# Performance work log

Hardware: AMD Instinct MI355X
Metric: run time of the kernel (lower is better)

## Reference

```python
import jax, jax.numpy as jnp
import numpy as np

B, T, N, FI = 2, 16, 256, 1
H, NHEAD, L = 64, 4, 2
MID, LOW, FOUT = 32, 16, 1


def layer_norm(x, g, b, eps=1e-5):
    m = jnp.mean(x, axis=-1, keepdims=True)
    v = jnp.var(x, axis=-1, keepdims=True)
    return (x - m) / jnp.sqrt(v + eps) * g + b


def setup_inputs() -> dict:
    key = jax.random.key(0)
    ks = jax.random.split(key, 24)
    s = 0.05
    inp = {
        'x_seq': jax.random.normal(ks[0], (B, T, N, FI), jnp.float32),
        'edge_index': jax.random.randint(ks[1], (2, 16), 0, N),
        'Wi': jax.random.normal(ks[2], (FI, H), jnp.float32) * s,
        'bi': jnp.zeros((H,), jnp.float32),
        'Wqkv': jax.random.normal(ks[3], (L, H, 3 * H), jnp.float32) * s,
        'bqkv': jnp.zeros((L, 3 * H), jnp.float32),
        'Wo': jax.random.normal(ks[4], (L, H, H), jnp.float32) * s,
        'bo': jnp.zeros((L, H), jnp.float32),
        'ln1_g': jnp.ones((L, H), jnp.float32),
        'ln1_b': jnp.zeros((L, H), jnp.float32),
        'W1': jax.random.normal(ks[5], (L, H, 4 * H), jnp.float32) * s,
        'b1': jnp.zeros((L, 4 * H), jnp.float32),
        'W2': jax.random.normal(ks[6], (L, 4 * H, H), jnp.float32) * s,
        'b2': jnp.zeros((L, H), jnp.float32),
        'ln2_g': jnp.ones((L, H), jnp.float32),
        'ln2_b': jnp.zeros((L, H), jnp.float32),
        'dW1': jax.random.normal(ks[7], (H, MID), jnp.float32) * s,
        'db1': jnp.zeros((MID,), jnp.float32),
        'dW2': jax.random.normal(ks[8], (MID, LOW), jnp.float32) * s,
        'db2': jnp.zeros((LOW,), jnp.float32),
        'dW3': jax.random.normal(ks[9], (LOW, FOUT), jnp.float32) * s,
        'db3': jnp.zeros((FOUT,), jnp.float32),
    }
    return inp


def reference(x_seq, edge_index, Wi, bi, Wqkv, bqkv, Wo, bo, ln1_g, ln1_b,
              W1, b1, W2, b2, ln2_g, ln2_b, dW1, db1, dW2, db2, dW3, db3):
    b, t, n, _ = x_seq.shape
    dh = H // NHEAD
    # input projection
    x = x_seq @ Wi + bi  # [B,T,N,H]
    # sinusoidal time positional encoding (broadcast over nodes)
    pos = jnp.arange(t, dtype=jnp.float32)[:, None]
    div = jnp.exp(jnp.arange(0, H, 2, dtype=jnp.float32) * (-jnp.log(10000.0) / H))
    tp = jnp.zeros((t, H), jnp.float32)
    tp = tp.at[:, 0::2].set(jnp.sin(pos * div)).at[:, 1::2].set(jnp.cos(pos * div))
    x = x + tp[None, :, None, :]
    S = t * n
    x = x.reshape(b, S, H)
    # block-causal additive bias: position i cannot attend to strictly future timesteps
    t_idx = jnp.arange(S) // n
    bias = jnp.where(t_idx[None, :] > t_idx[:, None], -jnp.inf, 0.0).astype(x.dtype)
    inv_sqrt_dh = 1.0 / jnp.sqrt(jnp.asarray(dh, x.dtype))
    for l in range(L):
        qkv = x @ Wqkv[l] + bqkv[l]  # [B,S,3H]
        q, k, v = jnp.split(qkv, 3, axis=-1)
        q = q.reshape(b, S, NHEAD, dh).transpose(0, 2, 1, 3)
        k = k.reshape(b, S, NHEAD, dh).transpose(0, 2, 1, 3)
        v = v.reshape(b, S, NHEAD, dh).transpose(0, 2, 1, 3)
        scores = jnp.einsum('bhqd,bhkd->bhqk', q, k) * inv_sqrt_dh + bias
        attn = jax.nn.softmax(scores, axis=-1)
        o = jnp.einsum('bhqk,bhkd->bhqd', attn, v)
        o = o.transpose(0, 2, 1, 3).reshape(b, S, H)
        o = o @ Wo[l] + bo[l]
        x = layer_norm(x + o, ln1_g[l], ln1_b[l])
        f = jax.nn.relu(x @ W1[l] + b1[l]) @ W2[l] + b2[l]
        x = layer_norm(x + f, ln2_g[l], ln2_b[l])
    last = x.reshape(b, t, n, H)[:, -1]  # [B,N,H]
    h = jax.nn.relu(last @ dW1 + db1)
    h = jax.nn.relu(h @ dW2 + db2)
    return h @ dW3 + db3  # [B,N,1]
```

## Files before the change

kernel.cpp:

```cpp
#include <hip/hip_runtime.h>
#include <math.h>


namespace {
constexpr int T_ = 16, N_ = 256, S_ = 4096;
constexpr int PAIRS = 136;

constexpr size_t OFF_A    = 0;
constexpr size_t OFF_BT   = 192;
constexpr size_t OFF_XB   = 3264;
constexpr size_t OFF_ALPH = 4288;
constexpr size_t OFF_BET  = 4292;
constexpr size_t OFF_GAM  = 4356;
constexpr size_t OFF_DELT = 4420;
constexpr size_t OFF_MN   = 5444;
constexpr size_t OFF_MX   = 5476;
constexpr size_t OFF_X    = 5632;
constexpr size_t OFF_QKV  = 529920;
constexpr size_t OFF_P0   = 2102784;
constexpr size_t OFF_PM1  = 3675648;
constexpr size_t OFF_PL1  = 3708416;
constexpr size_t OFF_PA1  = 3741184;
constexpr size_t OFF_WT   = 4265472;

typedef float  f32x16 __attribute__((ext_vector_type(16)));
typedef short  short8 __attribute__((ext_vector_type(8)));

__device__ inline float wave_sum(float v) {
#pragma unroll
  for (int off = 32; off > 0; off >>= 1) v += __shfl_xor(v, off, 64);
  return v;
}
__device__ inline unsigned bf16_rne(float f) {
  unsigned u = __float_as_uint(f);
  return (u + 0x7FFFu + ((u >> 16) & 1u)) >> 16;
}
__device__ inline unsigned pack2(float a, float b) {
  return bf16_rne(a) | (bf16_rne(b) << 16);
}
__device__ inline f32x16 zero16() {
  f32x16 z;
#pragma unroll
  for (int i = 0; i < 16; ++i) z[i] = 0.f;
  return z;
}
__device__ inline float pe_val(int t, int h) {
  float div = __expf((float)(h & ~1) * (-0.14391156831212787f));
  float arg = (float)t * div;
  return (h & 1) ? cosf(arg) : sinf(arg);
}
__device__ inline float rebuild(short h, short l) {
  return __uint_as_float(((unsigned)(unsigned short)h) << 16) +
         __uint_as_float(((unsigned)(unsigned short)l) << 16);
}
__device__ __forceinline__ void split4_store(short* hp, short* lp,
                                             float v0, float v1, float v2, float v3) {
  unsigned u0 = __float_as_uint(v0), u1 = __float_as_uint(v1);
  unsigned u2 = __float_as_uint(v2), u3 = __float_as_uint(v3);
  float r0 = v0 - __uint_as_float(u0 & 0xFFFF0000u);
  float r1 = v1 - __uint_as_float(u1 & 0xFFFF0000u);
  float r2 = v2 - __uint_as_float(u2 & 0xFFFF0000u);
  float r3 = v3 - __uint_as_float(u3 & 0xFFFF0000u);
  *(uint2*)hp = make_uint2((u0 >> 16) | (u1 & 0xFFFF0000u),
                           (u2 >> 16) | (u3 & 0xFFFF0000u));
  *(uint2*)lp = make_uint2(pack2(r0, r1), pack2(r2, r3));
}
__device__ __forceinline__ f32x16 gemm_tile(
    const short* __restrict__ Wh, const short* __restrict__ Wl, int tileRow,
    int inDim, int nkt, const short* Bh, const short* Bl, int bstride,
    int l31, int hi) {
  f32x16 C = zero16();
  for (int kt = 0; kt < nkt; ++kt) {
    int ko = kt * 16 + 8 * hi;
    short8 Ah = *(const short8*)&Wh[tileRow * inDim + ko];
    short8 Al = *(const short8*)&Wl[tileRow * inDim + ko];
    short8 Bh8 = *(const short8*)&Bh[l31 * bstride + ko];
    short8 Bl8 = *(const short8*)&Bl[l31 * bstride + ko];
    C = __builtin_amdgcn_mfma_f32_32x32x16_bf16(Ah, Bh8, C, 0, 0, 0);
    C = __builtin_amdgcn_mfma_f32_32x32x16_bf16(Al, Bh8, C, 0, 0, 0);
    C = __builtin_amdgcn_mfma_f32_32x32x16_bf16(Ah, Bl8, C, 0, 0, 0);
  }
  return C;
}

__global__ void k_setup(const float* __restrict__ x_seq,
                        const float* __restrict__ Wi, const float* __restrict__ bi,
                        const float* __restrict__ Wqkv, const float* __restrict__ bqkv,
                        const float* __restrict__ Wo, const float* __restrict__ W1,
                        const float* __restrict__ W2,
                        float* __restrict__ A, float* __restrict__ Bt,
                        float* __restrict__ Xb,
                        float* __restrict__ ALPH, float* __restrict__ BET,
                        float* __restrict__ GAM, float* __restrict__ DELT,
                        float* __restrict__ MN, float* __restrict__ MX,
                        short* __restrict__ WT) {
  int t = blockIdx.x, tid = threadIdx.x;
  if (t < 16) {
    if (tid < 192) {
      float acc = bqkv[tid];
#pragma unroll 8
      for (int h = 0; h < 64; ++h)
        acc = fmaf(bi[h] + pe_val(t, h), Wqkv[h * 192 + tid], acc);
      Bt[t * 192 + tid] = acc;
    }
    if (tid < 64) Xb[t * 64 + tid] = bi[tid] + pe_val(t, tid);
  } else if (t == 16) {
    if (tid < 192) {
      float acc = 0.f;
#pragma unroll 8
      for (int h = 0; h < 64; ++h) acc = fmaf(Wi[h], Wqkv[h * 192 + tid], acc);
      A[tid] = acc;
    }
  } else if (t == 17) {
    __shared__ float sA[128];
    __shared__ float sB[16][128];
    if (tid < 128) {
      float acc = 0.f;
#pragma unroll 8
      for (int h = 0; h < 64; ++h) acc = fmaf(Wi[h], Wqkv[h * 192 + tid], acc);
      sA[tid] = acc;
    }
    {
      int tt = tid >> 4, i = tid & 15;
      float accv[8];
#pragma unroll
      for (int j = 0; j < 8; ++j) accv[j] = bqkv[i * 8 + j];
      for (int h = 0; h < 64; ++h) {
        float xb = bi[h] + pe_val(tt, h);
#pragma unroll
        for (int j = 0; j < 8; ++j)
          accv[j] = fmaf(xb, Wqkv[h * 192 + i * 8 + j], accv[j]);
      }
#pragma unroll
      for (int j = 0; j < 8; ++j) sB[tt][i * 8 + j] = accv[j];
    }
    __syncthreads();
    const float k2 = 0.36067376022224085f;
    if (tid < 4) {
      float d = 0.f;
#pragma unroll
      for (int i = 0; i < 16; ++i) d = fmaf(sA[tid * 16 + i], sA[64 + tid * 16 + i], d);
      ALPH[tid] = k2 * d;
    }
    if (tid < 64) {
      int h = tid >> 4, tp2 = tid & 15;
      float d = 0.f, g = 0.f;
#pragma unroll
      for (int i = 0; i < 16; ++i) {
        d = fmaf(sA[h * 16 + i], sB[tp2][64 + h * 16 + i], d);
        g = fmaf(sA[64 + h * 16 + i], sB[tp2][h * 16 + i], g);
      }
      BET[h * 16 + tp2] = k2 * d;
      GAM[h * 16 + tp2] = k2 * g;
    }
#pragma unroll
    for (int q = 0; q < 4; ++q) {
      int idx = tid + 256 * q;
      int h = idx >> 8, ta = (idx >> 4) & 15, tb = idx & 15;
      float d = 0.f;
#pragma unroll
      for (int i = 0; i < 16; ++i)
        d = fmaf(sB[ta][h * 16 + i], sB[tb][64 + h * 16 + i], d);
      DELT[h * 256 + ta * 16 + tb] = k2 * d;
    }
  } else if (t == 18) {
    int g = tid >> 3, i = tid & 7;
    const float* xp = x_seq + (g >> 4) * S_ + (g & 15) * N_;
    float mn = 1e30f, mx = -1e30f;
    for (int j = i; j < 256; j += 8) {
      float v = xp[j];
      mn = fminf(mn, v); mx = fmaxf(mx, v);
    }
#pragma unroll
    for (int off = 1; off < 8; off <<= 1) {
      mn = fminf(mn, __shfl_xor(mn, off, 64));
      mx = fmaxf(mx, __shfl_xor(mx, off, 64));
    }
    if (i == 0) { MN[g] = mn; MX[g] = mx; }
  } else {
    int tb2 = t - 19;
    const float* Wq1 = Wqkv + 64 * 192;
#pragma unroll
    for (int e = 0; e < 4; ++e) {
      int gi = tb2 * 1024 + e * 256 + tid;
      float v; int hdst, ldst;
      if (gi < 4096) {
        int o = gi >> 6, i = gi & 63; v = Wo[i * 64 + o];
        hdst = gi; ldst = gi + 4096;
      } else if (gi < 20480) {
        int li = gi - 4096; int o = li >> 6, i = li & 63; v = W1[i * 256 + o];
        hdst = 8192 + li; ldst = 24576 + li;
      } else if (gi < 36864) {
        int li = gi - 20480; int o = li >> 8, i = li & 255; v = W2[i * 64 + o];
        hdst = 40960 + li; ldst = 57344 + li;
      } else {
        int li = gi - 36864; int o = li >> 6, i = li & 63; v = Wq1[i * 192 + o];
        hdst = 73728 + li; ldst = 86016 + li;
      }
      unsigned u = __float_as_uint(v);
      WT[hdst] = (short)(u >> 16);
      WT[ldst] = (short)bf16_rne(v - __uint_as_float(u & 0xFFFF0000u));
    }
  }
}

__global__ __launch_bounds__(256, 4) void k_attn0(
    const float* __restrict__ x_seq,
    const float* __restrict__ ALPH, const float* __restrict__ BET,
    const float* __restrict__ GAM, const float* __restrict__ DELT,
    const float* __restrict__ MN, const float* __restrict__ MX,
    float* __restrict__ P0) {
  __shared__ float4 xk4[64];
  int blk = blockIdx.x;
  int bh = blk / PAIRS, pair = blk % PAIRS;
  int b = bh >> 2, h = bh & 3;
  int tq = 0, p = pair;
  while (p >= tq + 1) { p -= tq + 1; ++tq; }
  int kt = p;
  int tid = threadIdx.x;
  if (tid < 64) xk4[tid] = *(const float4*)(x_seq + (size_t)(b * S_ + kt * N_) + 4 * tid);
  __syncthreads();

  float x = x_seq[b * S_ + tq * N_ + tid];
  float a = fmaf(ALPH[h], x, GAM[h * 16 + tq]);
  float xext = (a >= 0.f) ? MX[b * 16 + kt] : MN[b * 16 + kt];
  float axext = a * xext;
  float Mg = axext + fmaf(BET[h * 16 + kt], x, DELT[h * 256 + tq * 16 + kt]);
  float sp0 = 0.f, sp1 = 0.f, sp2 = 0.f, sp3 = 0.f;
  float sx0 = 0.f, sx1 = 0.f, sx2 = 0.f, sx3 = 0.f;
#pragma unroll 8
  for (int j = 0; j < 64; ++j) {
    float4 xv = xk4[j];
    float e0 = __builtin_amdgcn_exp2f(fmaf(a, xv.x, -axext));
    float e1 = __builtin_amdgcn_exp2f(fmaf(a, xv.y, -axext));
    float e2 = __builtin_amdgcn_exp2f(fmaf(a, xv.z, -axext));
    float e3 = __builtin_amdgcn_exp2f(fmaf(a, xv.w, -axext));
    sp0 += e0; sp1 += e1; sp2 += e2; sp3 += e3;
    sx0 = fmaf(xv.x, e0, sx0); sx1 = fmaf(xv.y, e1, sx1);
    sx2 = fmaf(xv.z, e2, sx2); sx3 = fmaf(xv.w, e3, sx3);
  }
  size_t pb = ((size_t)(bh * 16 + tq) * 16 + kt) * 768;
  P0[pb + tid]       = Mg;
  P0[pb + 256 + tid] = (sp0 + sp1) + (sp2 + sp3);
  P0[pb + 512 + tid] = (sx0 + sx1) + (sx2 + sx3);
}

__global__ __launch_bounds__(256, 2) void k_fused0(
    const float* __restrict__ P0, const float* __restrict__ A,
    const float* __restrict__ Bt, const float* __restrict__ Xb,
    const float* __restrict__ x_seq, const float* __restrict__ Wi,
    const float* __restrict__ bo, const float* __restrict__ g1,
    const float* __restrict__ be1, const float* __restrict__ bb1,
    const float* __restrict__ bb2, const float* __restrict__ g2,
    const float* __restrict__ be2, const float* __restrict__ bq1,
    const short* __restrict__ WT,
    float* __restrict__ X, float* __restrict__ QKV) {
  __shared__ short qbh[32][72], qbl[32][72];
  __shared__ short xsh[32][72], xsl[32][72];
  __shared__ short hsh[32][264], hsl[32][264];
  __shared__ float ys[16][68];

  const short* WoTh = WT;          const short* WoTl = WT + 4096;
  const short* W1Th = WT + 8192;   const short* W1Tl = WT + 24576;
  const short* W2Th = WT + 40960;  const short* W2Tl = WT + 57344;
  const short* WqTh = WT + 73728;  const short* WqTl = WT + 86016;

  int blk = blockIdx.x;
  int b = blk >> 8, t = (blk >> 4) & 15, n0 = (blk & 15) * 16;
  int gbase = b * S_ + t * N_ + n0;
  int tid = threadIdx.x;
  int w = tid >> 6, lane = tid & 63, l31 = lane & 31, hi = lane >> 5;

  for (int i = tid; i < 16 * 72; i += 256) {
    (&qbh[16][0])[i] = 0; (&qbl[16][0])[i] = 0;
    (&xsh[16][0])[i] = 0; (&xsl[16][0])[i] = 0;
  }
  for (int i = tid; i < 16 * 264; i += 256) {
    (&hsh[16][0])[i] = 0; (&hsl[16][0])[i] = 0;
  }

  {
    int r = tid & 15, hh = (tid >> 4) & 3, d4 = tid >> 6;
    int n = n0 + r, bh4 = b * 4 + hh;
    size_t pbase = ((size_t)(bh4 * 16 + t) * 16) * 768 + n;
    float M = -INFINITY;
    for (int kt = 0; kt <= t; ++kt)
      M = fmaxf(M, P0[pbase + (size_t)kt * 768]);
    float D = 0.f, SX = 0.f, c0 = 0.f, c1 = 0.f, c2 = 0.f, c3 = 0.f;
    for (int kt = 0; kt <= t; ++kt) {
      size_t pb = pbase + (size_t)kt * 768;
      float wgt = __builtin_amdgcn_exp2f(P0[pb] - M);
      float wsp = wgt * P0[pb + 256];
      D += wsp;
      SX = fmaf(wgt, P0[pb + 512], SX);
      float4 bv = *(const float4*)(Bt + kt * 192 + 128 + hh * 16 + d4 * 4);
      c0 = fmaf(wsp, bv.x, c0); c1 = fmaf(wsp, bv.y, c1);
      c2 = fmaf(wsp, bv.z, c2); c3 = fmaf(wsp, bv.w, c3);
    }
    float invD = 1.f / D;
    float4 av = *(const float4*)(A + 128 + hh * 16 + d4 * 4);
    float o0 = fmaf(SX, av.x, c0) * invD;
    float o1 = fmaf(SX, av.y, c1) * invD;
    float o2 = fmaf(SX, av.z, c2) * invD;
    float o3 = fmaf(SX, av.w, c3) * invD;
    split4_store(&qbh[r][hh * 16 + d4 * 4], &qbl[r][hh * 16 + d4 * 4],
                 o0, o1, o2, o3);
  }
  __syncthreads();

  if (w < 2) {
    f32x16 C = gemm_tile(WoTh, WoTl, w * 32 + l31, 64, 4,
                         &qbh[0][0], &qbl[0][0], 72, l31, hi);
    if (l31 < 16) {
#pragma unroll
      for (int g = 0; g < 4; ++g)
        *(float4*)&ys[l31][w * 32 + g * 8 + 4 * hi] =
            make_float4(C[4 * g], C[4 * g + 1], C[4 * g + 2], C[4 * g + 3]);
    }
  }
  __syncthreads();

  {
    int c = tid & 63, grp = tid >> 6;
    float xb_c = Xb[t * 64 + c], wi_c = Wi[c], bo_c = bo[c];
    float g1c = g1[c], be1c = be1[c];
#pragma unroll
    for (int rr = 0; rr < 4; ++rr) {
      int row = grp * 4 + rr;
      float xv = x_seq[gbase + row];
      float val = ys[row][c] + bo_c + fmaf(xv, wi_c, xb_c);
      float mean = wave_sum(val) * (1.f / 64.f);
      float dv = val - mean;
      float var = wave_sum(dv * dv) * (1.f / 64.f);
      float xn = dv * rsqrtf(var + 1e-5f) * g1c + be1c;
      unsigned u = __float_as_uint(xn);
      xsh[row][c] = (short)(u >> 16);
      xsl[row][c] = (short)bf16_rne(xn - __uint_as_float(u & 0xFFFF0000u));
    }
  }
  __syncthreads();

#pragma unroll
  for (int ti = 0; ti < 2; ++ti) {
    int tt = w + 4 * ti;
    f32x16 C = gemm_tile(W1Th, W1Tl, tt * 32 + l31, 64, 4,
                         &xsh[0][0], &xsl[0][0], 72, l31, hi);
    if (l31 < 16) {
#pragma unroll
      for (int g = 0; g < 4; ++g) {
        int cb = tt * 32 + g * 8 + 4 * hi;
        float v0 = fmaxf(C[4 * g + 0] + bb1[cb + 0], 0.f);
        float v1 = fmaxf(C[4 * g + 1] + bb1[cb + 1], 0.f);
        float v2 = fmaxf(C[4 * g + 2] + bb1[cb + 2], 0.f);
        float v3 = fmaxf(C[4 * g + 3] + bb1[cb + 3], 0.f);
        split4_store(&hsh[l31][cb], &hsl[l31][cb], v0, v1, v2, v3);
      }
    }
  }
  __syncthreads();

  if (w < 2) {
    f32x16 C = gemm_tile(W2Th, W2Tl, w * 32 + l31, 256, 16,
                         &hsh[0][0], &hsl[0][0], 264, l31, hi);
    if (l31 < 16) {
#pragma unroll
      for (int g = 0; g < 4; ++g)
        *(float4*)&ys[l31][w * 32 + g * 8 + 4 * hi] =
            make_float4(C[4 * g], C[4 * g + 1], C[4 * g + 2], C[4 * g + 3]);
    }
  }
  __syncthreads();

  {
    int c = tid & 63, grp = tid >> 6;
    float b2c = bb2[c], g2c = g2[c], be2c = be2[c];
#pragma unroll
    for (int rr = 0; rr < 4; ++rr) {
      int row = grp * 4 + rr;
      float val = ys[row][c] + b2c + rebuild(xsh[row][c], xsl[row][c]);
      float mean = wave_sum(val) * (1.f / 64.f);
      float dv = val - mean;
      float var = wave_sum(dv * dv) * (1.f / 64.f);
      float xn = dv * rsqrtf(var + 1e-5f) * g2c + be2c;
      unsigned u = __float_as_uint(xn);
      qbh[row][c] = (short)(u >> 16);
      qbl[row][c] = (short)bf16_rne(xn - __uint_as_float(u & 0xFFFF0000u));
      if (t == 15) X[(size_t)(gbase + row) * 64 + c] = xn;
    }
  }
  __syncthreads();

  {
    int tlA = (t == 15) ? w : (2 + w);
    int ntl = (t == 15 && w < 2) ? 2 : 1;
    for (int ti = 0; ti < ntl; ++ti) {
      int tt = ti ? (w + 4) : tlA;
      f32x16 C = gemm_tile(WqTh, WqTl, tt * 32 + l31, 64, 4,
                           &qbh[0][0], &qbl[0][0], 72, l31, hi);
      if (l31 < 16) {
        size_t rb = (size_t)(gbase + l31) * 192;
#pragma unroll
        for (int g = 0; g < 4; ++g) {
          int cb = tt * 32 + g * 8 + 4 * hi;
          float4 o = make_float4(C[4 * g + 0] + bq1[cb + 0],
                                 C[4 * g + 1] + bq1[cb + 1],
                                 C[4 * g + 2] + bq1[cb + 2],
                                 C[4 * g + 3] + bq1[cb + 3]);
          *(float4*)&QKV[rb + cb] = o;
        }
      }
    }
  }
}

__global__ __launch_bounds__(256, 4) void k_attn1(const float* __restrict__ QKV,
    float* __restrict__ PM, float* __restrict__ PL, float* __restrict__ PACC) {
  __shared__ short KH[2][256][8];
  __shared__ short KL[2][256][8];
  __shared__ short VT[32][264];
  int blk = blockIdx.x;
  int bh = blk >> 4, kt = blk & 15;
  const int tq = 15;
  int b = bh >> 2, h = bh & 3;
  int tid = threadIdx.x, w = tid >> 6, lane = tid & 63;
  int l31 = lane & 31, hi = lane >> 5;
  const size_t qkvbase = (size_t)b * S_ * 192;

  for (int i = tid; i < 16 * 264; i += 256) (&VT[16][0])[i] = 0;
  {
    const float* kp = QKV + qkvbase + (size_t)(kt * N_ + tid) * 192 + 64 + h * 16;
    float kf[16], vf[16];
#pragma unroll
    for (int i = 0; i < 4; ++i) {
      float4 k4 = *(const float4*)(kp + 4 * i);
      kf[4 * i] = k4.x; kf[4 * i + 1] = k4.y; kf[4 * i + 2] = k4.z; kf[4 * i + 3] = k4.w;
      float4 v4 = *(const float4*)(kp + 64 + 4 * i);
      vf[4 * i] = v4.x; vf[4 * i + 1] = v4.y; vf[4 * i + 2] = v4.z; vf[4 * i + 3] = v4.w;
    }
    short8 kh0, kh1, kl0, kl1;
#pragma unroll
    for (int i = 0; i < 8; ++i) {
      unsigned ht0 = __float_as_uint(kf[i]) & 0xFFFF0000u;
      kh0[i] = (short)(ht0 >> 16);
      kl0[i] = (short)bf16_rne(kf[i] - __uint_as_float(ht0));
      unsigned ht1 = __float_as_uint(kf[i + 8]) & 0xFFFF0000u;
      kh1[i] = (short)(ht1 >> 16);
      kl1[i] = (short)bf16_rne(kf[i + 8] - __uint_as_float(ht1));
    }
    *(short8*)&KH[0][tid][0] = kh0;
    *(short8*)&KH[1][tid][0] = kh1;
    *(short8*)&KL[0][tid][0] = kl0;
    *(short8*)&KL[1][tid][0] = kl1;
#pragma unroll
    for (int i = 0; i < 16; ++i) VT[i][tid] = (short)bf16_rne(vf[i]);
  }
  __syncthreads();

  const float cscale = 0.36067376022224085f;
  short8 Qh[2], Ql[2];
#pragma unroll
  for (int qs = 0; qs < 2; ++qs) {
    int qloc = w * 64 + qs * 32 + l31;
    const float* qp = QKV + qkvbase + (size_t)(tq * N_ + qloc) * 192 + h * 16 + 8 * hi;
    float4 a4 = *(const float4*)(qp), b4 = *(const float4*)(qp + 4);
    float qf[8] = {a4.x, a4.y, a4.z, a4.w, b4.x, b4.y, b4.z, b4.w};
#pragma unroll
    for (int i = 0; i < 8; ++i) {
      float q = qf[i] * cscale;
      unsigned ht = __float_as_uint(q) & 0xFFFF0000u;
      Qh[qs][i] = (short)(ht >> 16);
      Ql[qs][i] = (short)bf16_rne(q - __uint_as_float(ht));
    }
  }

  f32x16 O0 = zero16(), O1 = zero16();
  float m[2] = {-INFINITY, -INFINITY}, lsum[2] = {0.f, 0.f};

  for (int ks = 0; ks < 8; ++ks) {
    const short8 Kh = *(const short8*)&KH[hi][ks * 32 + l31][0];
    const short8 Kl = *(const short8*)&KL[hi][ks * 32 + l31][0];
    const short8 Va = *(const short8*)&VT[l31][ks * 32 + 8 * hi];
    const short8 Vb = *(const short8*)&VT[l31][ks * 32 + 8 * hi + 16];

#pragma unroll
    for (int qs = 0; qs < 2; ++qs) {
      f32x16 S = zero16();
      S = __builtin_amdgcn_mfma_f32_32x32x16_bf16(Kh, Qh[qs], S, 0, 0, 0);
      S = __builtin_amdgcn_mfma_f32_32x32x16_bf16(Kl, Qh[qs], S, 0, 0, 0);
      S = __builtin_amdgcn_mfma_f32_32x32x16_bf16(Kh, Ql[qs], S, 0, 0, 0);

      float pm = S[0];
#pragma unroll
      for (int r = 1; r < 16; ++r) pm = fmaxf(pm, S[r]);
      pm = fmaxf(pm, __shfl_xor(pm, 32, 64));
      float mq = m[qs];
      if (__any(pm > mq)) {
        float mn = fmaxf(mq, pm);
        float al = __builtin_amdgcn_exp2f(mq - mn);
        m[qs] = mn; mq = mn;
        lsum[qs] *= al;
        if (qs == 0) {
#pragma unroll
          for (int r = 0; r < 16; ++r) O0[r] *= al;
        } else {
#pragma unroll
          for (int r = 0; r < 16; ++r) O1[r] *= al;
        }
      }
      float pr[16], ps = 0.f;
#pragma unroll
      for (int r = 0; r < 16; ++r) {
        pr[r] = __builtin_amdgcn_exp2f(S[r] - mq);
        ps += pr[r];
      }
      lsum[qs] += ps + __shfl_xor(ps, 32, 64);

      unsigned w01 = pack2(pr[0],  pr[1]);
      unsigned w23 = pack2(pr[2],  pr[3]);
      unsigned w45 = pack2(pr[4],  pr[5]);
      unsigned w67 = pack2(pr[6],  pr[7]);
      unsigned w89 = pack2(pr[8],  pr[9]);
      unsigned wab = pack2(pr[10], pr[11]);
      unsigned wcd = pack2(pr[12], pr[13]);
      unsigned wef = pack2(pr[14], pr[15]);
      unsigned e01 = __shfl_xor(w01, 32, 64), e23 = __shfl_xor(w23, 32, 64);
      unsigned e45 = __shfl_xor(w45, 32, 64), e67 = __shfl_xor(w67, 32, 64);
      unsigned e89 = __shfl_xor(w89, 32, 64), eab = __shfl_xor(wab, 32, 64);
      unsigned ecd = __shfl_xor(wcd, 32, 64), eef = __shfl_xor(wef, 32, 64);
      union { short8 s; unsigned u[4]; } P0u, P1u;
      P0u.u[0] = hi ? e45 : w01;
      P0u.u[1] = hi ? e67 : w23;
      P0u.u[2] = hi ? w45 : e01;
      P0u.u[3] = hi ? w67 : e23;
      P1u.u[0] = hi ? ecd : w89;
      P1u.u[1] = hi ? eef : wab;
      P1u.u[2] = hi ? wcd : e89;
      P1u.u[3] = hi ? wef : eab;

      if (qs == 0) {
        O0 = __builtin_amdgcn_mfma_f32_32x32x16_bf16(Va, P0u.s, O0, 0, 0, 0);
        O0 = __builtin_amdgcn_mfma_f32_32x32x16_bf16(Vb, P1u.s, O0, 0, 0, 0);
      } else {
        O1 = __builtin_amdgcn_mfma_f32_32x32x16_bf16(Va, P0u.s, O1, 0, 0, 0);
        O1 = __builtin_amdgcn_mfma_f32_32x32x16_bf16(Vb, P1u.s, O1, 0, 0, 0);
      }
    }
  }

  int slot = blk;
#pragma unroll
  for (int qs = 0; qs < 2; ++qs) {
    int qloc = w * 64 + qs * 32 + l31;
    if (lane < 32) {
      PM[(size_t)slot * 256 + qloc] = m[qs];
      PL[(size_t)slot * 256 + qloc] = lsum[qs];
    }
    float* pa = PACC + (size_t)slot * 4096 + (size_t)qloc * 16;
    float4 lo4, hi4;
    if (qs == 0) {
      lo4 = make_float4(O0[0], O0[1], O0[2], O0[3]);
      hi4 = make_float4(O0[4], O0[5], O0[6], O0[7]);
    } else {
      lo4 = make_float4(O1[0], O1[1], O1[2], O1[3]);
      hi4 = make_float4(O1[4], O1[5], O1[6], O1[7]);
    }
    *(float4*)(pa + 4 * hi)     = lo4;
    *(float4*)(pa + 8 + 4 * hi) = hi4;
  }
}

__global__ __launch_bounds__(256, 2) void k_fused1(
    const float* __restrict__ PM1, const float* __restrict__ PL1,
    const float* __restrict__ PA1,
    const float* __restrict__ Wo, const float* __restrict__ bo,
    const float* __restrict__ g1, const float* __restrict__ be1,
    const float* __restrict__ W1, const float* __restrict__ bb1,
    const float* __restrict__ W2, const float* __restrict__ bb2,
    const float* __restrict__ g2, const float* __restrict__ be2,
    const float* __restrict__ X,
    const float* __restrict__ dW1, const float* __restrict__ db1,
    const float* __restrict__ dW2, const float* __restrict__ db2,
    const float* __restrict__ dW3, const float* __restrict__ db3,
    float* __restrict__ out) {
  __shared__ float os[4][64], rs[4][64], xs[4][64], x2[4][64], hs[4][256];
  __shared__ float h1s[4][32], h2s[4][16];
  int tid = threadIdx.x;
  int bb = blockIdx.x >> 6;
  int nbase = (blockIdx.x & 63) * 4;
  int row0 = bb * S_ + 15 * N_ + nbase;
  size_t base = (size_t)row0 * 64;

  {
    int d = tid & 15, r = (tid >> 4) & 3, h = tid >> 6;
    int n = nbase + r;
    int sb = (bb * 4 + h) * 16;
    float M = -INFINITY;
#pragma unroll
    for (int s = 0; s < 16; ++s) M = fmaxf(M, PM1[(size_t)(sb + s) * 256 + n]);
    float D = 0.f, od = 0.f;
#pragma unroll
    for (int s = 0; s < 16; ++s) {
      float wgt = __builtin_amdgcn_exp2f(PM1[(size_t)(sb + s) * 256 + n] - M);
      D = fmaf(PL1[(size_t)(sb + s) * 256 + n], wgt, D);
      od = fmaf(PA1[(size_t)(sb + s) * 4096 + (size_t)n * 16 + d], wgt, od);
    }
    os[r][h * 16 + d] = od / D;
    rs[tid >> 6][tid & 63] = X[base + tid];
  }
  __syncthreads();

  int c = tid & 63, grp = tid >> 6;
  {
    float a = bo[c];
#pragma unroll 8
    for (int k = 0; k < 64; ++k) a = fmaf(os[grp][k], Wo[k * 64 + c], a);
    float val = a + rs[grp][c];
    float mean = wave_sum(val) * (1.f / 64.f);
    float dv = val - mean;
    float var = wave_sum(dv * dv) * (1.f / 64.f);
    xs[grp][c] = dv * rsqrtf(var + 1e-5f) * g1[c] + be1[c];
  }
  __syncthreads();

  {
    float am0 = bb1[tid], am1 = am0, am2 = am0, am3 = am0;
    for (int k4 = 0; k4 < 16; ++k4) {
      float w0 = W1[(4 * k4 + 0) * 256 + tid];
      float w1v = W1[(4 * k4 + 1) * 256 + tid];
      float w2v = W1[(4 * k4 + 2) * 256 + tid];
      float w3v = W1[(4 * k4 + 3) * 256 + tid];
      float4 x0 = *(const float4*)&xs[0][4 * k4];
      float4 x1 = *(const float4*)&xs[1][4 * k4];
      float4 x2v = *(const float4*)&xs[2][4 * k4];
      float4 x3 = *(const float4*)&xs[3][4 * k4];
      am0 = fmaf(x0.x, w0, am0); am0 = fmaf(x0.y, w1v, am0);
      am0 = fmaf(x0.z, w2v, am0); am0 = fmaf(x0.w, w3v, am0);
      am1 = fmaf(x1.x, w0, am1); am1 = fmaf(x1.y, w1v, am1);
      am1 = fmaf(x1.z, w2v, am1); am1 = fmaf(x1.w, w3v, am1);
      am2 = fmaf(x2v.x, w0, am2); am2 = fmaf(x2v.y, w1v, am2);
      am2 = fmaf(x2v.z, w2v, am2); am2 = fmaf(x2v.w, w3v, am2);
      am3 = fmaf(x3.x, w0, am3); am3 = fmaf(x3.y, w1v, am3);
      am3 = fmaf(x3.z, w2v, am3); am3 = fmaf(x3.w, w3v, am3);
    }
    hs[0][tid] = fmaxf(am0, 0.f);
    hs[1][tid] = fmaxf(am1, 0.f);
    hs[2][tid] = fmaxf(am2, 0.f);
    hs[3][tid] = fmaxf(am3, 0.f);
  }
  __syncthreads();

  {
    float a = bb2[c];
    for (int k4 = 0; k4 < 64; ++k4) {
      float w0 = W2[(4 * k4 + 0) * 64 + c];
      float w1v = W2[(4 * k4 + 1) * 64 + c];
      float w2v = W2[(4 * k4 + 2) * 64 + c];
      float w3v = W2[(4 * k4 + 3) * 64 + c];
      float4 hv = *(const float4*)&hs[grp][4 * k4];
      a = fmaf(hv.x, w0, a); a = fmaf(hv.y, w1v, a);
      a = fmaf(hv.z, w2v, a); a = fmaf(hv.w, w3v, a);
    }
    float val = a + xs[grp][c];
    float mean = wave_sum(val) * (1.f / 64.f);
    float dv = val - mean;
    float var = wave_sum(dv * dv) * (1.f / 64.f);
    x2[grp][c] = dv * rsqrtf(var + 1e-5f) * g2[c] + be2[c];
  }
  __syncthreads();

  if (tid < 128) {
    int r = tid >> 5, mid = tid & 31;
    float a = db1[mid];
#pragma unroll 8
    for (int k = 0; k < 64; ++k) a = fmaf(x2[r][k], dW1[k * 32 + mid], a);
    h1s[r][mid] = fmaxf(a, 0.f);
  }
  __syncthreads();
  if (tid < 64) {
    int r = tid >> 4, low = tid & 15;
    float a = db2[low];
#pragma unroll
    for (int k = 0; k < 32; ++k) a = fmaf(h1s[r][k], dW2[k * 16 + low], a);
    h2s[r][low] = fmaxf(a, 0.f);
  }
  __syncthreads();
  if (tid < 4) {
    float a = db3[0];
#pragma unroll
    for (int k = 0; k < 16; ++k) a = fmaf(h2s[tid][k], dW3[k], a);
    out[bb * 256 + nbase + tid] = a;
  }
}

}

extern "C" void kernel_launch(void* const* d_in, const int* in_sizes, int n_in,
                              void* d_out, int out_size, void* d_ws, size_t ws_size,
                              hipStream_t stream) {
  const float* x_seq = (const float*)d_in[0];
  const float* Wi   = (const float*)d_in[2];
  const float* bi   = (const float*)d_in[3];
  const float* Wqkv = (const float*)d_in[4];
  const float* bqkv = (const float*)d_in[5];
  const float* Wo   = (const float*)d_in[6];
  const float* bo   = (const float*)d_in[7];
  const float* ln1g = (const float*)d_in[8];
  const float* ln1b = (const float*)d_in[9];
  const float* W1   = (const float*)d_in[10];
  const float* b1   = (const float*)d_in[11];
  const float* W2   = (const float*)d_in[12];
  const float* b2   = (const float*)d_in[13];
  const float* ln2g = (const float*)d_in[14];
  const float* ln2b = (const float*)d_in[15];
  const float* dW1  = (const float*)d_in[16];
  const float* db1  = (const float*)d_in[17];
  const float* dW2  = (const float*)d_in[18];
  const float* db2  = (const float*)d_in[19];
  const float* dW3  = (const float*)d_in[20];
  const float* db3  = (const float*)d_in[21];

  float* ws   = (float*)d_ws;
  float* A    = ws + OFF_A;
  float* Bt   = ws + OFF_BT;
  float* Xb   = ws + OFF_XB;
  float* ALPH = ws + OFF_ALPH;
  float* BET  = ws + OFF_BET;
  float* GAM  = ws + OFF_GAM;
  float* DELT = ws + OFF_DELT;
  float* MN   = ws + OFF_MN;
  float* MX   = ws + OFF_MX;
  float* X    = ws + OFF_X;
  float* QKV  = ws + OFF_QKV;
  float* P0   = ws + OFF_P0;
  float* PM1  = ws + OFF_PM1;
  float* PL1  = ws + OFF_PL1;
  float* PA1  = ws + OFF_PA1;
  short* WT   = (short*)(ws + OFF_WT);

  k_setup<<<67, 256, 0, stream>>>(x_seq, Wi, bi, Wqkv, bqkv, Wo, W1, W2,
                                  A, Bt, Xb, ALPH, BET, GAM, DELT, MN, MX, WT);
  k_attn0<<<8 * PAIRS, 256, 0, stream>>>(x_seq, ALPH, BET, GAM, DELT, MN, MX, P0);
  k_fused0<<<512, 256, 0, stream>>>(P0, A, Bt, Xb, x_seq, Wi,
                                    bo, ln1g, ln1b, b1, b2, ln2g, ln2b,
                                    bqkv + 192, WT, X, QKV);
  k_attn1<<<128, 256, 0, stream>>>(QKV, PM1, PL1, PA1);
  k_fused1<<<128, 256, 0, stream>>>(PM1, PL1, PA1,
                                    Wo + 4096, bo + 64, ln1g + 64, ln1b + 64,
                                    W1 + 64 * 256, b1 + 256, W2 + 256 * 64, b2 + 64,
                                    ln2g + 64, ln2b + 64, X,
                                    dW1, db1, dW2, db2, dW3, db3, (float*)d_out);
}
```

Before: 86.24 us.

## Fuse setup kernel into layer-0 attention kernel by recomputing per-block scalars

Removes the separate setup launch by folding its weight-transpose and bias work into extra blocks of the layer-0 attention kernel. Each attention block now computes its own alpha/beta/gamma/delta coefficients and key min/max in-block, instead of reading them from a precomputed workspace. This drops one kernel launch and its dependency barrier. In exchange every attention block does redundant 64-step dot products and extra syncs.

```diff
diff --git a/kernel.cpp b/kernel.cpp
--- a/kernel.cpp
+++ b/kernel.cpp
@@ -9,12 +9,6 @@
 constexpr size_t OFF_A    = 0;
 constexpr size_t OFF_BT   = 192;
 constexpr size_t OFF_XB   = 3264;
-constexpr size_t OFF_ALPH = 4288;
-constexpr size_t OFF_BET  = 4292;
-constexpr size_t OFF_GAM  = 4356;
-constexpr size_t OFF_DELT = 4420;
-constexpr size_t OFF_MN   = 5444;
-constexpr size_t OFF_MX   = 5476;
 constexpr size_t OFF_X    = 5632;
 constexpr size_t OFF_QKV  = 529920;
 constexpr size_t OFF_P0   = 2102784;
@@ -83,149 +77,128 @@
   return C;
 }
 
-__global__ void k_setup(const float* __restrict__ x_seq,
-                        const float* __restrict__ Wi, const float* __restrict__ bi,
-                        const float* __restrict__ Wqkv, const float* __restrict__ bqkv,
-                        const float* __restrict__ Wo, const float* __restrict__ W1,
-                        const float* __restrict__ W2,
-                        float* __restrict__ A, float* __restrict__ Bt,
-                        float* __restrict__ Xb,
-                        float* __restrict__ ALPH, float* __restrict__ BET,
-                        float* __restrict__ GAM, float* __restrict__ DELT,
-                        float* __restrict__ MN, float* __restrict__ MX,
-                        short* __restrict__ WT) {
-  int t = blockIdx.x, tid = threadIdx.x;
-  if (t < 16) {
-    if (tid < 192) {
-      float acc = bqkv[tid];
+__global__ __launch_bounds__(256, 4) void k_attn0s(
+    const float* __restrict__ x_seq, const float* __restrict__ Wi,
+    const float* __restrict__ bi, const float* __restrict__ Wqkv,
+    const float* __restrict__ bqkv, const float* __restrict__ Wo,
+    const float* __restrict__ W1, const float* __restrict__ W2,
+    float* __restrict__ A, float* __restrict__ Bt, float* __restrict__ Xb,
+    short* __restrict__ WT, float* __restrict__ P0) {
+  int blk = blockIdx.x, tid = threadIdx.x;
+
+  if (blk >= 8 * PAIRS) {
+    int t = blk - 8 * PAIRS;
+    if (t < 16) {
+      if (tid < 192) {
+        float acc = bqkv[tid];
 #pragma unroll 8
-      for (int h = 0; h < 64; ++h)
-        acc = fmaf(bi[h] + pe_val(t, h), Wqkv[h * 192 + tid], acc);
-      Bt[t * 192 + tid] = acc;
-    }
-    if (tid < 64) Xb[t * 64 + tid] = bi[tid] + pe_val(t, tid);
-  } else if (t == 16) {
-    if (tid < 192) {
-      float acc = 0.f;
+        for (int h = 0; h < 64; ++h)
+          acc = fmaf(bi[h] + pe_val(t, h), Wqkv[h * 192 + tid], acc);
+        Bt[t * 192 + tid] = acc;
+      }
+      if (tid < 64) Xb[t * 64 + tid] = bi[tid] + pe_val(t, tid);
+    } else if (t == 16) {
+      if (tid < 192) {
+        float acc = 0.f;
 #pragma unroll 8
-      for (int h = 0; h < 64; ++h) acc = fmaf(Wi[h], Wqkv[h * 192 + tid], acc);
-      A[tid] = acc;
-    }
-  } else if (t == 17) {
-    __shared__ float sA[128];
-    __shared__ float sB[16][128];
-    if (tid < 128) {
-      float acc = 0.f;
-#pragma unroll 8
-      for (int h = 0; h < 64; ++h) acc = fmaf(Wi[h], Wqkv[h * 192 + tid], acc);
-      sA[tid] = acc;
-    }
-    {
-      int tt = tid >> 4, i = tid & 15;
-      float accv[8];
-#pragma unroll
-      for (int j = 0; j < 8; ++j) accv[j] = bqkv[i * 8 + j];
-      for (int h = 0; h < 64; ++h) {
-        float xb = bi[h] + pe_val(tt, h);
-#pragma unroll
-        for (int j = 0; j < 8; ++j)
-          accv[j] = fmaf(xb, Wqkv[h * 192 + i * 8 + j], accv[j]);
-      }
-#pragma unroll
-      for (int j = 0; j < 8; ++j) sB[tt][i * 8 + j] = accv[j];
-    }
-    __syncthreads();
-    const float k2 = 0.36067376022224085f;
-    if (tid < 4) {
-      float d = 0.f;
-#pragma unroll
-      for (int i = 0; i < 16; ++i) d = fmaf(sA[tid * 16 + i], sA[64 + tid * 16 + i], d);
-      ALPH[tid] = k2 * d;
-    }
-    if (tid < 64) {
-      int h = tid >> 4, tp2 = tid & 15;
-      float d = 0.f, g = 0.f;
-#pragma unroll
-      for (int i = 0; i < 16; ++i) {
-        d = fmaf(sA[h * 16 + i], sB[tp2][64 + h * 16 + i], d);
-        g = fmaf(sA[64 + h * 16 + i], sB[tp2][h * 16 + i], g);
-      }
-      BET[h * 16 + tp2] = k2 * d;
-      GAM[h * 16 + tp2] = k2 * g;
-    }
-#pragma unroll
-    for (int q = 0; q < 4; ++q) {
-      int idx = tid + 256 * q;
-      int h = idx >> 8, ta = (idx >> 4) & 15, tb = idx & 15;
-      float d = 0.f;
-#pragma unroll
-      for (int i = 0; i < 16; ++i)
-        d = fmaf(sB[ta][h * 16 + i], sB[tb][64 + h * 16 + i], d);
-      DELT[h * 256 + ta * 16 + tb] = k2 * d;
-    }
-  } else if (t == 18) {
-    int g = tid >> 3, i = tid & 7;
-    const float* xp = x_seq + (g >> 4) * S_ + (g & 15) * N_;
-    float mn = 1e30f, mx = -1e30f;
-    for (int j = i; j < 256; j += 8) {
-      float v = xp[j];
-      mn = fminf(mn, v); mx = fmaxf(mx, v);
-    }
-#pragma unroll
-    for (int off = 1; off < 8; off <<= 1) {
-      mn = fminf(mn, __shfl_xor(mn, off, 64));
-      mx = fmaxf(mx, __shfl_xor(mx, off, 64));
-    }
-    if (i == 0) { MN[g] = mn; MX[g] = mx; }
-  } else {
-    int tb2 = t - 19;
-    const float* Wq1 = Wqkv + 64 * 192;
-#pragma unroll
-    for (int e = 0; e < 4; ++e) {
-      int gi = tb2 * 1024 + e * 256 + tid;
-      float v; int hdst, ldst;
-      if (gi < 4096) {
-        int o = gi >> 6, i = gi & 63; v = Wo[i * 64 + o];
-        hdst = gi; ldst = gi + 4096;
-      } else if (gi < 20480) {
-        int li = gi - 4096; int o = li >> 6, i = li & 63; v = W1[i * 256 + o];
-        hdst = 8192 + li; ldst = 24576 + li;
-      } else if (gi < 36864) {
-        int li = gi - 20480; int o = li >> 8, i = li & 255; v = W2[i * 64 + o];
-        hdst = 40960 + li; ldst = 57344 + li;
-      } else {
-        int li = gi - 36864; int o = li >> 6, i = li & 63; v = Wq1[i * 192 + o];
-        hdst = 73728 + li; ldst = 86016 + li;
-      }
-      unsigned u = __float_as_uint(v);
-      WT[hdst] = (short)(u >> 16);
-      WT[ldst] = (short)bf16_rne(v - __uint_as_float(u & 0xFFFF0000u));
-    }
-  }
-}
-
-__global__ __launch_bounds__(256, 4) void k_attn0(
-    const float* __restrict__ x_seq,
-    const float* __restrict__ ALPH, const float* __restrict__ BET,
-    const float* __restrict__ GAM, const float* __restrict__ DELT,
-    const float* __restrict__ MN, const float* __restrict__ MX,
-    float* __restrict__ P0) {
+        for (int h = 0; h < 64; ++h) acc = fmaf(Wi[h], Wqkv[h * 192 + tid], acc);
+        A[tid] = acc;
+      }
+    } else {
+      int tb2 = t - 17;
+      const float* Wq1 = Wqkv + 64 * 192;
+#pragma unroll
+      for (int e = 0; e < 4; ++e) {
+        int gi = tb2 * 1024 + e * 256 + tid;
+        float v; int hdst, ldst;
+        if (gi < 4096) {
+          int o = gi >> 6, i = gi & 63; v = Wo[i * 64 + o];
+          hdst = gi; ldst = gi + 4096;
+        } else if (gi < 20480) {
+          int li = gi - 4096; int o = li >> 6, i = li & 63; v = W1[i * 256 + o];
+          hdst = 8192 + li; ldst = 24576 + li;
+        } else if (gi < 36864) {
+          int li = gi - 20480; int o = li >> 8, i = li & 255; v = W2[i * 64 + o];
+          hdst = 40960 + li; ldst = 57344 + li;
+        } else {
+          int li = gi - 36864; int o = li >> 6, i = li & 63; v = Wq1[i * 192 + o];
+          hdst = 73728 + li; ldst = 86016 + li;
+        }
+        unsigned u = __float_as_uint(v);
+        WT[hdst] = (short)(u >> 16);
+        WT[ldst] = (short)bf16_rne(v - __uint_as_float(u & 0xFFFF0000u));
+      }
+    }
+    return;
+  }
+
   __shared__ float4 xk4[64];
-  int blk = blockIdx.x;
+  __shared__ float peq[64], pek[64];
+  __shared__ float red[8];
+  __shared__ float scal[6];
+
   int bh = blk / PAIRS, pair = blk % PAIRS;
   int b = bh >> 2, h = bh & 3;
   int tq = 0, p = pair;
   while (p >= tq + 1) { p -= tq + 1; ++tq; }
   int kt = p;
-  int tid = threadIdx.x;
-  if (tid < 64) xk4[tid] = *(const float4*)(x_seq + (size_t)(b * S_ + kt * N_) + 4 * tid);
+
+  if (tid < 64)
+    xk4[tid] = *(const float4*)(x_seq + (size_t)(b * S_ + kt * N_) + 4 * tid);
+  else if (tid < 128)
+    peq[tid - 64] = bi[tid - 64] + pe_val(tq, tid - 64);
+  else if (tid < 192)
+    pek[tid - 128] = bi[tid - 128] + pe_val(kt, tid - 128);
+  __syncthreads();
+
+  {
+    float xv = ((const float*)xk4)[tid];
+    float mn = xv, mx = xv;
+#pragma unroll
+    for (int off = 32; off > 0; off >>= 1) {
+      mn = fminf(mn, __shfl_xor(mn, off, 64));
+      mx = fmaxf(mx, __shfl_xor(mx, off, 64));
+    }
+    if ((tid & 63) == 0) { red[tid >> 6] = mn; red[4 + (tid >> 6)] = mx; }
+  }
+  {
+    float aq = 0.f, ak = 0.f, bq = 0.f, bk = 0.f;
+    if (tid < 16) {
+      int cq = h * 16 + tid, ck = 64 + h * 16 + tid;
+#pragma unroll 8
+      for (int hh = 0; hh < 64; ++hh) {
+        float wq = Wqkv[hh * 192 + cq], wk = Wqkv[hh * 192 + ck];
+        aq = fmaf(Wi[hh], wq, aq);
+        ak = fmaf(Wi[hh], wk, ak);
+        bq = fmaf(peq[hh], wq, bq);
+        bk = fmaf(pek[hh], wk, bk);
+      }
+      bq += bqkv[cq]; bk += bqkv[ck];
+    }
+    float pa = aq * ak, pb = aq * bk, pg = ak * bq, pd = bq * bk;
+#pragma unroll
+    for (int off = 8; off > 0; off >>= 1) {
+      pa += __shfl_xor(pa, off, 64);
+      pb += __shfl_xor(pb, off, 64);
+      pg += __shfl_xor(pg, off, 64);
+      pd += __shfl_xor(pd, off, 64);
+    }
+    __syncthreads();
+    if (tid == 0) {
+      const float k2 = 0.36067376022224085f;
+      scal[0] = k2 * pa; scal[1] = k2 * pb;
+      scal[2] = k2 * pg; scal[3] = k2 * pd;
+      scal[4] = fminf(fminf(red[0], red[1]), fminf(red[2], red[3]));
+      scal[5] = fmaxf(fmaxf(red[4], red[5]), fmaxf(red[6], red[7]));
+    }
+  }
   __syncthreads();
 
   float x = x_seq[b * S_ + tq * N_ + tid];
-  float a = fmaf(ALPH[h], x, GAM[h * 16 + tq]);
-  float xext = (a >= 0.f) ? MX[b * 16 + kt] : MN[b * 16 + kt];
+  float a = fmaf(scal[0], x, scal[2]);
+  float xext = (a >= 0.f) ? scal[5] : scal[4];
   float axext = a * xext;
-  float Mg = axext + fmaf(BET[h * 16 + kt], x, DELT[h * 256 + tq * 16 + kt]);
+  float Mg = axext + fmaf(scal[1], x, scal[3]);
   float sp0 = 0.f, sp1 = 0.f, sp2 = 0.f, sp3 = 0.f;
   float sx0 = 0.f, sx1 = 0.f, sx2 = 0.f, sx3 = 0.f;
 #pragma unroll 8
@@ -239,10 +212,10 @@
     sx0 = fmaf(xv.x, e0, sx0); sx1 = fmaf(xv.y, e1, sx1);
     sx2 = fmaf(xv.z, e2, sx2); sx3 = fmaf(xv.w, e3, sx3);
   }
-  size_t pb = ((size_t)(bh * 16 + tq) * 16 + kt) * 768;
-  P0[pb + tid]       = Mg;
-  P0[pb + 256 + tid] = (sp0 + sp1) + (sp2 + sp3);
-  P0[pb + 512 + tid] = (sx0 + sx1) + (sx2 + sx3);
+  size_t pb2 = ((size_t)(bh * 16 + tq) * 16 + kt) * 768;
+  P0[pb2 + tid]       = Mg;
+  P0[pb2 + 256 + tid] = (sp0 + sp1) + (sp2 + sp3);
+  P0[pb2 + 512 + tid] = (sx0 + sx1) + (sx2 + sx3);
 }
 
 __global__ __launch_bounds__(256, 2) void k_fused0(
@@ -723,12 +696,6 @@
   float* A    = ws + OFF_A;
   float* Bt   = ws + OFF_BT;
   float* Xb   = ws + OFF_XB;
-  float* ALPH = ws + OFF_ALPH;
-  float* BET  = ws + OFF_BET;
-  float* GAM  = ws + OFF_GAM;
-  float* DELT = ws + OFF_DELT;
-  float* MN   = ws + OFF_MN;
-  float* MX   = ws + OFF_MX;
   float* X    = ws + OFF_X;
   float* QKV  = ws + OFF_QKV;
   float* P0   = ws + OFF_P0;
@@ -737,9 +704,8 @@
   float* PA1  = ws + OFF_PA1;
   short* WT   = (short*)(ws + OFF_WT);
 
-  k_setup<<<67, 256, 0, stream>>>(x_seq, Wi, bi, Wqkv, bqkv, Wo, W1, W2,
-                                  A, Bt, Xb, ALPH, BET, GAM, DELT, MN, MX, WT);
-  k_attn0<<<8 * PAIRS, 256, 0, stream>>>(x_seq, ALPH, BET, GAM, DELT, MN, MX, P0);
+  k_attn0s<<<8 * PAIRS + 65, 256, 0, stream>>>(x_seq, Wi, bi, Wqkv, bqkv,
+                                               Wo, W1, W2, A, Bt, Xb, WT, P0);
   k_fused0<<<512, 256, 0, stream>>>(P0, A, Bt, Xb, x_seq, Wi,
                                     bo, ln1g, ln1b, b1, b2, ln2g, ln2b,
                                     bqkv + 192, WT, X, QKV);
```

Result: faster. 72.23 us (-16.2%).
